# Performance work log

Hardware: AMD Instinct MI355X
Metric: run time of the kernel (lower is better)

Reference implementation:

```python
import jax, jax.numpy as jnp
import numpy as np

DIM = 64  # module-level global `dim` used as the softmax scale


def setup_inputs() -> dict:
    key = jax.random.key(0)
    kq, kk, kv, km = jax.random.split(key, 4)
    B, H, S, d = 4, 16, 2048, DIM
    Q = jax.random.normal(kq, (B, H, S, d), dtype=jnp.float32)
    K = jax.random.normal(kk, (B, H, S, d), dtype=jnp.float32)
    V = jax.random.normal(kv, (B, H, S, d), dtype=jnp.float32)
    attn_mask = jax.random.randint(km, (B, H, S, S), 0, 2).astype(jnp.bool_)
    return {"Q": Q, "K": K, "V": V, "attn_mask": attn_mask}


def reference(Q, K, V, attn_mask):
    scale = 1.0 / np.sqrt(DIM).astype(np.float32)
    # scores: [B, H, S, S]
    scores = jnp.einsum("bhqd,bhkd->bhqk", Q, K) * scale
    # NOTE: original torch code does masked_fill_(attn_mask, 0) — fills with 0, not -inf
    scores = jnp.where(attn_mask, jnp.zeros((), scores.dtype), scores)
    attn = jax.nn.softmax(scores, axis=-1)
    context = jnp.einsum("bhqk,bhkd->bhqd", attn, V)
    return context
```

## Files before the change

kernel.cpp:

```cpp
#include <hip/hip_runtime.h>
#include <hip/hip_bf16.h>

typedef __bf16 bf16;
typedef __attribute__((ext_vector_type(8))) __bf16 bf16x8;
typedef __attribute__((ext_vector_type(4))) __bf16 bf16x4;
typedef __attribute__((ext_vector_type(4))) float f32x4;
typedef __attribute__((ext_vector_type(4))) int i32x4;
typedef __attribute__((ext_vector_type(4))) short s16x4;

constexpr int SLEN = 2048;
constexpr int DH = 64;
constexpr int NBH = 64;
constexpr float SCALE_LOG2E = 0.125f * 1.4426950408889634f;

__global__ __launch_bounds__(256) void prep_kv_kernel(
    const float* __restrict__ K, const float* __restrict__ V,
    bf16* __restrict__ Kb, bf16* __restrict__ Vt)
{
    __shared__ float t[64][65];
    const int bh = blockIdx.y;
    const int s0 = blockIdx.x * 64;
    const int tx = threadIdx.x & 63, ty = threadIdx.x >> 6;

    const float* vp = V + ((size_t)bh * SLEN + s0) * DH;
    #pragma unroll
    for (int r = ty; r < 64; r += 4) t[r][tx] = vp[(size_t)r * DH + tx];

    {
        const float* kp = K + ((size_t)bh * SLEN + s0) * DH;
        bf16* kbp = Kb + ((size_t)bh * SLEN + s0) * DH;
        int r = threadIdx.x >> 2, c = (threadIdx.x & 3) * 16;
        const float4* src = (const float4*)(kp + (size_t)r * DH + c);
        float4 a = src[0], b = src[1], c2 = src[2], d = src[3];
        bf16x8 o0, o1;
        o0[0]=(bf16)a.x;  o0[1]=(bf16)a.y;  o0[2]=(bf16)a.z;  o0[3]=(bf16)a.w;
        o0[4]=(bf16)b.x;  o0[5]=(bf16)b.y;  o0[6]=(bf16)b.z;  o0[7]=(bf16)b.w;
        o1[0]=(bf16)c2.x; o1[1]=(bf16)c2.y; o1[2]=(bf16)c2.z; o1[3]=(bf16)c2.w;
        o1[4]=(bf16)d.x;  o1[5]=(bf16)d.y;  o1[6]=(bf16)d.z;  o1[7]=(bf16)d.w;
        *(bf16x8*)(kbp + (size_t)r * DH + c)     = o0;
        *(bf16x8*)(kbp + (size_t)r * DH + c + 8) = o1;
    }

    __syncthreads();
    bf16* op = Vt + (size_t)bh * DH * SLEN + s0;
    #pragma unroll
    for (int r = ty; r < 64; r += 4) op[(size_t)r * SLEN + tx] = (bf16)t[tx][r];
}

__device__ __forceinline__ void gl_lds16(const void* g, void* l) {
    __builtin_amdgcn_global_load_lds(
        (const __attribute__((address_space(1))) void*)g,
        (__attribute__((address_space(3))) void*)l, 16, 0, 0);
}

__device__ __forceinline__ f32x4 pv_mfma(bf16x4 a, bf16x4 b, f32x4 c) {
#if __has_builtin(__builtin_amdgcn_mfma_f32_16x16x16bf16_1k)
    return __builtin_amdgcn_mfma_f32_16x16x16bf16_1k(
        __builtin_bit_cast(s16x4, a), __builtin_bit_cast(s16x4, b), c, 0, 0, 0);
#else
    f32x4 d;
    asm("s_nop 1\n\t"
        "v_mfma_f32_16x16x16_bf16 %0, %1, %2, %3\n\t"
        "s_nop 7"
        : "=v"(d) : "v"(a), "v"(b), "v"(c));
    return d;
#endif
}

__global__ __launch_bounds__(256, 4) void attn_kernel(
    const float* __restrict__ Q, const int* __restrict__ mask,
    const bf16* __restrict__ Kb, const bf16* __restrict__ Vtb,
    float* __restrict__ out)
{
    __shared__ char KT[2][8192];
    __shared__ char VT[2][8192];

    const int h = blockIdx.x;
    const int logical = (h & 7) * 256 + (h >> 3);
    const int bh = logical >> 5;
    const int qbase = (logical & 31) * 64;
    const int tid = threadIdx.x;
    const int w = tid >> 6, l = tid & 63;
    const int lq = l & 15, lg = l >> 4;

    const char* kgb = (const char*)(Kb + (size_t)bh * SLEN * DH);
    const char* vgb = (const char*)(Vtb + (size_t)bh * DH * SLEN);

    const int kv_r = l >> 3;
    const int kv_c = ((l & 7) * 16) ^ (kv_r << 4);

    bf16x8 aq[2];
    {
        const float* qp = Q + ((size_t)bh * SLEN + qbase + w * 16 + lq) * DH + lg * 8;
        #pragma unroll
        for (int t = 0; t < 2; ++t) {
            float4 x = *(const float4*)(qp + t * 32);
            float4 y = *(const float4*)(qp + t * 32 + 4);
            bf16x8 f;
            f[0]=(bf16)x.x; f[1]=(bf16)x.y; f[2]=(bf16)x.z; f[3]=(bf16)x.w;
            f[4]=(bf16)y.x; f[5]=(bf16)y.y; f[6]=(bf16)y.z; f[7]=(bf16)y.w;
            aq[t] = f;
        }
    }

    f32x4 acc[4] = {{0,0,0,0},{0,0,0,0},{0,0,0,0},{0,0,0,0}};
    float dpart = 0.f;
    const int swzk = (lq & 7) << 4;

    const int* mrow = mask + ((size_t)bh * SLEN + qbase + w * 16 + lq) * SLEN;

    auto stage = [&](int t, int buf) {
        const int kb = t * 64;
        #pragma unroll
        for (int q = 0; q < 2; ++q) {
            int r = (w * 2 + q) * 8 + kv_r;
            gl_lds16(kgb + (size_t)(kb + r) * 128 + kv_c, &KT[buf][(w * 2 + q) * 1024]);
            gl_lds16(vgb + (size_t)r * 4096 + (size_t)kb * 2 + kv_c, &VT[buf][(w * 2 + q) * 1024]);
        }
    };
    auto loadmask = [&](int t, i32x4* m) {
        #pragma unroll
        for (int n = 0; n < 4; ++n)
            m[n] = __builtin_nontemporal_load((const i32x4*)(mrow + t * 64 + n * 16 + lg * 4));
    };
    auto body = [&](int cur, const i32x4* mC) {
        bf16x4 p[4];
        #pragma unroll
        for (int n = 0; n < 4; ++n) {
            f32x4 s = {0, 0, 0, 0};
            #pragma unroll
            for (int t = 0; t < 2; ++t) {
                bf16x8 bk = *(const bf16x8*)&KT[cur][(n * 16 + lq) * 128 + ((t * 64 + lg * 16) ^ swzk)];
                s = __builtin_amdgcn_mfma_f32_16x16x32_bf16(bk, aq[t], s, 0, 0, 0);
            }
            #pragma unroll
            for (int i = 0; i < 4; ++i) {
                float e = mC[n][i] ? 0.0f : s[i] * SCALE_LOG2E;
                float pe = exp2f(e);
                dpart += pe;
                p[n][i] = (bf16)pe;
            }
        }
        #pragma unroll
        for (int nn = 0; nn < 4; ++nn) {
            #pragma unroll
            for (int n = 0; n < 4; ++n) {
                bf16x4 bv = *(const bf16x4*)&VT[cur][(nn * 16 + lq) * 128 + ((n * 32 + lg * 8) ^ swzk)];
                acc[nn] = pv_mfma(p[n], bv, acc[nn]);
            }
        }
    };
    auto tile_sync = [&]() {
        asm volatile("s_waitcnt vmcnt(4) lgkmcnt(0)" ::: "memory");
        __builtin_amdgcn_s_barrier();
        __builtin_amdgcn_sched_barrier(0);
    };

    i32x4 mA[4], mB[4];

    stage(0, 0);
    __builtin_amdgcn_sched_barrier(0);
    loadmask(0, mA);
    tile_sync();

    for (int kt = 0; kt < SLEN / 64; kt += 2) {
        stage(kt + 1, 1);
        __builtin_amdgcn_sched_barrier(0);
        loadmask(kt + 1, mB);
        body(0, mA);
        tile_sync();

        const bool more = (kt + 2) < (SLEN / 64);
        if (more) {
            stage(kt + 2, 0);
            __builtin_amdgcn_sched_barrier(0);
            loadmask(kt + 2, mA);
        }
        body(1, mB);
        if (more) tile_sync();
    }

    dpart += __shfl_xor(dpart, 16, 64);
    dpart += __shfl_xor(dpart, 32, 64);
    float dinv = 1.0f / dpart;

    float di[4];
    #pragma unroll
    for (int i = 0; i < 4; ++i) di[i] = __shfl(dinv, lg * 4 + i, 64);

    float* op = out + ((size_t)bh * SLEN + qbase + w * 16) * DH;
    #pragma unroll
    for (int n = 0; n < 4; ++n) {
        #pragma unroll
        for (int i = 0; i < 4; ++i)
            op[(size_t)(lg * 4 + i) * DH + n * 16 + lq] = acc[n][i] * di[i];
    }
}

extern "C" void kernel_launch(void* const* d_in, const int* in_sizes, int n_in,
                              void* d_out, int out_size, void* d_ws, size_t ws_size,
                              hipStream_t stream) {
    const float* Q    = (const float*)d_in[0];
    const float* K    = (const float*)d_in[1];
    const float* V    = (const float*)d_in[2];
    const int*   mask = (const int*)d_in[3];
    float* out = (float*)d_out;

    bf16* Kb  = (bf16*)d_ws;
    bf16* Vtb = Kb + (size_t)NBH * SLEN * DH;

    prep_kv_kernel<<<dim3(SLEN / 64, NBH), 256, 0, stream>>>(K, V, Kb, Vtb);
    attn_kernel<<<2048, 256, 0, stream>>>(Q, mask, Kb, Vtb, out);
}
```

Measured before the change: 314.2 us.

## Pack mask into bitmasks, single-buffer mask registers, raise occupancy target

Rather than holding two full i32x4[4] mask register sets (mA/mB) live across the unrolled two-tile loop, the mask for the current tile is compressed into four 4-bit words before the next tile's raw mask load is issued. The loop becomes a single-tile iteration with a toggled LDS buffer index, and launch bounds go from 4 to 5 waves per SIMD target to exploit the lower register pressure. Masked scores now compute exp2 unconditionally and select 1.0. The risks are less latency hiding for mask loads and possible spills under the tighter register budget.

```diff
diff --git a/kernel.cpp b/kernel.cpp
--- a/kernel.cpp
+++ b/kernel.cpp
@@ -11,6 +11,7 @@
 constexpr int SLEN = 2048;
 constexpr int DH = 64;
 constexpr int NBH = 64;
+constexpr int NT = SLEN / 64;
 constexpr float SCALE_LOG2E = 0.125f * 1.4426950408889634f;
 
 __global__ __launch_bounds__(256) void prep_kv_kernel(
@@ -67,7 +68,7 @@
 #endif
 }
 
-__global__ __launch_bounds__(256, 4) void attn_kernel(
+__global__ __launch_bounds__(256, 5) void attn_kernel(
     const float* __restrict__ Q, const int* __restrict__ mask,
     const bf16* __restrict__ Kb, const bf16* __restrict__ Vtb,
     float* __restrict__ out)
@@ -123,7 +124,7 @@
         for (int n = 0; n < 4; ++n)
             m[n] = __builtin_nontemporal_load((const i32x4*)(mrow + t * 64 + n * 16 + lg * 4));
     };
-    auto body = [&](int cur, const i32x4* mC) {
+    auto body = [&](int cur, const unsigned* pm) {
         bf16x4 p[4];
         #pragma unroll
         for (int n = 0; n < 4; ++n) {
@@ -135,8 +136,8 @@
             }
             #pragma unroll
             for (int i = 0; i < 4; ++i) {
-                float e = mC[n][i] ? 0.0f : s[i] * SCALE_LOG2E;
-                float pe = exp2f(e);
+                float pe = exp2f(s[i] * SCALE_LOG2E);
+                pe = ((pm[n] >> i) & 1u) ? 1.0f : pe;
                 dpart += pe;
                 p[n][i] = (bf16)pe;
             }
@@ -156,28 +157,27 @@
         __builtin_amdgcn_sched_barrier(0);
     };
 
-    i32x4 mA[4], mB[4];
+    i32x4 raw[4];
+    unsigned pm[4];
 
     stage(0, 0);
     __builtin_amdgcn_sched_barrier(0);
-    loadmask(0, mA);
+    loadmask(0, raw);
     tile_sync();
 
-    for (int kt = 0; kt < SLEN / 64; kt += 2) {
-        stage(kt + 1, 1);
+    int cur = 0;
+    for (int kt = 0; kt < NT; ++kt) {
+        const bool more = (kt + 1) < NT;
+        if (more) stage(kt + 1, cur ^ 1);
         __builtin_amdgcn_sched_barrier(0);
-        loadmask(kt + 1, mB);
-        body(0, mA);
-        tile_sync();
-
-        const bool more = (kt + 2) < (SLEN / 64);
-        if (more) {
-            stage(kt + 2, 0);
-            __builtin_amdgcn_sched_barrier(0);
-            loadmask(kt + 2, mA);
-        }
-        body(1, mB);
-        if (more) tile_sync();
+        #pragma unroll
+        for (int n = 0; n < 4; ++n)
+            pm[n] = (raw[n][0] != 0 ? 1u : 0u) | (raw[n][1] != 0 ? 2u : 0u)
+                  | (raw[n][2] != 0 ? 4u : 0u) | (raw[n][3] != 0 ? 8u : 0u);
+        if (more) loadmask(kt + 1, raw);
+        __builtin_amdgcn_sched_barrier(0);
+        body(cur, pm);
+        if (more) { tile_sync(); cur ^= 1; }
     }
 
     dpart += __shfl_xor(dpart, 16, 64);
```

Result: faster. 305.6 us, median of 2 (-2.7%).
